# Kernel tuning notes

Hardware: AMD Instinct MI355X
Metric: run time of the kernel (lower is better)

## Reference

```python
import jax, jax.numpy as jnp
import numpy as np

KS = 4
STRIDE = 2
PAD = 1
PI = 3.14  # module uses 3.14, not math.pi


def gabor_filters(freq, theta, psi, sigma):
    # freq/theta/psi/sigma: [O, I] -> weight [O, I, KS, KS]
    x0 = float(np.ceil(KS / 2))  # 2.0 for KS=4
    lin = jnp.linspace(-x0 + 1.0, x0, KS)  # [-1, 0, 1, 2]
    y = lin[:, None]  # varies along kernel dim 0 (meshgrid 'ij')
    x = lin[None, :]  # varies along kernel dim 1
    f = freq[..., None, None]
    t = theta[..., None, None]
    p = psi[..., None, None]
    s = sigma[..., None, None]
    rotx = x * jnp.cos(t) + y * jnp.sin(t)
    roty = -x * jnp.sin(t) + y * jnp.cos(t)
    g = jnp.exp(-0.5 * (rotx ** 2 + roty ** 2) / (s + 0.001) ** 2)
    g = g * jnp.cos(f * rotx + p)
    return g / (2.0 * PI * s ** 2)


def setup_inputs() -> dict:
    key = jax.random.key(0)
    ks = jax.random.split(key, 5)
    B, I, O, H, W = 32, 64, 128, 128, 128
    x = jax.random.normal(ks[0], (B, I, H, W), dtype=jnp.float32)
    # parameter init mirroring the torch module
    freq = (PI / 2) * 1.41 ** (-jax.random.randint(ks[1], (O, I), 0, 5).astype(jnp.float32))
    theta = (PI / 8) * jax.random.randint(ks[2], (O, I), 0, 8).astype(jnp.float32)
    psi = PI * jax.random.uniform(ks[3], (O, I), dtype=jnp.float32)
    sigma = PI / freq
    gamma = jnp.ones((O,), dtype=jnp.float32)
    beta = jnp.zeros((O,), dtype=jnp.float32)
    return {"x": x, "freq": freq, "theta": theta, "psi": psi,
            "sigma": sigma, "gamma": gamma, "beta": beta}


def reference(x, freq, theta, psi, sigma, gamma, beta):
    w = gabor_filters(freq, theta, psi, sigma)  # [O, I, 4, 4]
    out = jax.lax.conv_general_dilated(
        x, w, window_strides=(STRIDE, STRIDE),
        padding=[(PAD, PAD), (PAD, PAD)],
        dimension_numbers=("NCHW", "OIHW", "NCHW"))
    # BatchNorm2d in training mode: batch stats over (N, H, W), eps=1e-5
    mean = jnp.mean(out, axis=(0, 2, 3), keepdims=True)
    var = jnp.var(out, axis=(0, 2, 3), keepdims=True)
    xhat = (out - mean) * jax.lax.rsqrt(var + 1e-5)
    out = gamma[None, :, None, None] * xhat + beta[None, :, None, None]
    # LeakyReLU(0.1)
    return jnp.where(out >= 0, out, 0.1 * out)
```

## Files before the change

kernel.cpp:

```cpp
#include <hip/hip_runtime.h>
#include <hip/hip_bf16.h>

#define BATCH 32
#define CIN   64
#define COUT  128
#define HIN   128
#define WIN   128
#define HOUT  64
#define WOUT  64

typedef unsigned int u32;
typedef __attribute__((ext_vector_type(8))) short short8;
typedef __attribute__((ext_vector_type(4))) float f32x4;


__device__ inline unsigned short f2bf(float v) {
  __hip_bfloat16 h = __float2bfloat16(v);
  return *reinterpret_cast<unsigned short*>(&h);
}
__device__ inline u32 pack2(float a, float b) {
  return (u32)f2bf(a) | ((u32)f2bf(b) << 16);
}

__global__ __launch_bounds__(256) void gabor_kernel(
    const float* __restrict__ freq, const float* __restrict__ theta,
    const float* __restrict__ psi,  const float* __restrict__ sigma,
    __hip_bfloat16* __restrict__ wsw) {
  int idx = blockIdx.x * 256 + threadIdx.x;
  int o = idx >> 6, i = idx & 63;
  float f = freq[idx], t = theta[idx], p = psi[idx], s = sigma[idx];
  float ct = cosf(t), st = sinf(t);
  float se = s + 0.001f;
  float gsc = -0.5f / (se * se);
  float nrm = 1.0f / (2.0f * 3.14f * s * s);
  const float lin[4] = {-1.f, 0.f, 1.f, 2.f};
  int chunk = i >> 2;
  #pragma unroll
  for (int ky = 0; ky < 4; ++ky) {
    #pragma unroll
    for (int kx = 0; kx < 4; ++kx) {
      float xx = lin[kx], yy = lin[ky];
      float rx =  xx * ct + yy * st;
      float ry = -xx * st + yy * ct;
      float g = __expf(gsc * (rx * rx + ry * ry)) * cosf(f * rx + p) * nrm;
      int k6 = (i & 3) * 16 + ky * 4 + kx;
      int sub = 4 * (k6 >> 5) + ((k6 >> 3) & 3);
      int j = k6 & 7;
      int slot = sub ^ (o & 7);
      wsw[(chunk * 16384 + o * 128 + slot * 16 + j * 2) >> 1] = __float2bfloat16(g);
    }
  }
}

constexpr int XPITCH = 70;
constexpr int XROWS  = 18;
constexpr int XCH    = 1260;
constexpr int XBYTES = 20160;
constexpr int NSLOT  = 2304;

__global__ __launch_bounds__(1024, 4) void conv_mfma(
    const float* __restrict__ x, const char* __restrict__ wsW,
    float* __restrict__ out, float2* __restrict__ part) {
  __shared__ __align__(16) char lds[73088];

  const int tid = threadIdx.x;
  const int l = tid & 63, w = tid >> 6;
  const int wm = w & 1, wn = w >> 1;
  const int t4 = l >> 4, lcol = l & 15;
  const int khp = t4 & 1, ihalf = t4 >> 1;
  const int ohb = blockIdx.x, b = blockIdx.y;
  const int oh0 = ohb * 8;

  bool act[3]; int xbyte[3]; const float* gp[3];
  #pragma unroll
  for (int u = 0; u < 3; ++u) {
    int sg = tid + u * 1024;
    int r = sg >> 5, s = sg & 31;
    int ch = r / XROWS, row = r - ch * XROWS;
    int ih = oh0 * 2 - 1 + row;
    act[u] = (sg < NSLOT) && ((unsigned)ih < 128u);
    xbyte[u] = (ch * XCH + row * XPITCH) * 4 + s * 8;
    gp[u] = x + (((size_t)(b * 64 + ch) << 14) + (size_t)ih * 128 + 4 * s);
  }

  float4 xv[3];
  auto XLOAD = [&](int c) {
    #pragma unroll
    for (int u = 0; u < 3; ++u)
      if (act[u]) xv[u] = *(const float4*)(gp[u] + (size_t)c * 65536);
  };
  auto XWRITE = [&](int nb) {
    char* X = lds + 32768 + nb * XBYTES;
    #pragma unroll
    for (int u = 0; u < 3; ++u)
      if (act[u]) {
        char* pb = X + xbyte[u];
        *(unsigned short*)(pb + 6)  = f2bf(xv[u].x);
        *(u32*)(pb + 8)             = pack2(xv[u].y, xv[u].z);
        *(unsigned short*)(pb + 12) = f2bf(xv[u].w);
      }
  };

  auto ASTAGE = [&](int c, int nb) {
    const char* src = wsW + c * 16384 + w * 1024 + l * 16;
    char* dst = lds + nb * 16384 + w * 1024;
    __builtin_amdgcn_global_load_lds(
        (const __attribute__((address_space(1))) u32*)src,
        (__attribute__((address_space(3))) u32*)dst, 16, 0, 0);
  };

  {
    u32* X = (u32*)(lds + 32768);
    for (int i = tid; i < 2 * XBYTES / 4; i += 1024) X[i] = 0;
  }

  f32x4 acc[4][4];
  #pragma unroll
  for (int mf = 0; mf < 4; ++mf)
    #pragma unroll
    for (int nf = 0; nf < 4; ++nf) acc[mf][nf] = {0.f, 0.f, 0.f, 0.f};

  int bo[4];
  #pragma unroll
  for (int nf = 0; nf < 4; ++nf) {
    int nfb = 4 * wn + nf;
    bo[nf] = ihalf * XCH + khp * (2 * XPITCH) + lcol + 1 +
             (nfb >> 2) * (2 * XPITCH) + ((nfb & 3) << 4);
  }

  int ao[4][2];
  #pragma unroll
  for (int mf = 0; mf < 4; ++mf)
    #pragma unroll
    for (int kk = 0; kk < 2; ++kk)
      ao[mf][kk] = (wm * 64 + mf * 16 + lcol) * 128 +
                   (((4 * kk + t4) ^ (lcol & 7)) << 4);

  auto COMPUTE = [&](int cb) {
    const char* Ab = lds + cb * 16384;
    const u32* Xb = (const u32*)(lds + 32768 + cb * XBYTES);
    __builtin_amdgcn_s_setprio(1);
    #pragma unroll
    for (int kk = 0; kk < 2; ++kk) {
      short8 af[4];
      #pragma unroll
      for (int mf = 0; mf < 4; ++mf)
        af[mf] = *(const short8*)(Ab + ao[mf][kk]);
      #pragma unroll
      for (int nf = 0; nf < 4; ++nf) {
        const u32* p = Xb + bo[nf] + kk * (2 * XCH);
        union { u32 u[4]; short8 s8; } bu;
        bu.u[0] = p[0]; bu.u[1] = p[1];
        bu.u[2] = p[XPITCH]; bu.u[3] = p[XPITCH + 1];
        short8 bf = bu.s8;
        #pragma unroll
        for (int mf = 0; mf < 4; ++mf)
          acc[mf][nf] = __builtin_amdgcn_mfma_f32_16x16x32_bf16(af[mf], bf, acc[mf][nf], 0, 0, 0);
      }
    }
    __builtin_amdgcn_s_setprio(0);
  };

  ASTAGE(0, 0); XLOAD(0);
  __syncthreads();
  XWRITE(0);
  __syncthreads();
  for (int c = 0; c < 16; ++c) {
    int cur = c & 1;
    if (c < 15) { ASTAGE(c + 1, cur ^ 1); XLOAD(c + 1); }
    COMPUTE(cur);
    if (c < 15) XWRITE(cur ^ 1);
    __syncthreads();
  }

  size_t obase = ((size_t)b * 128) * 4096;
  #pragma unroll
  for (int mf = 0; mf < 4; ++mf)
    #pragma unroll
    for (int nf = 0; nf < 4; ++nf) {
      int nfb = 4 * wn + nf;
      int oh = oh0 + (nfb >> 2), ow = ((nfb & 3) << 4) + lcol;
      #pragma unroll
      for (int r = 0; r < 4; ++r) {
        int o = wm * 64 + mf * 16 + t4 * 4 + r;
        out[obase + (size_t)o * 4096 + oh * 64 + ow] = acc[mf][nf][r];
      }
    }

  float* ps = (float*)lds;
  #pragma unroll
  for (int mf = 0; mf < 4; ++mf)
    #pragma unroll
    for (int r = 0; r < 4; ++r) {
      float s1 = 0.f, s2 = 0.f;
      #pragma unroll
      for (int nf = 0; nf < 4; ++nf) { float v = acc[mf][nf][r]; s1 += v; s2 += v * v; }
      #pragma unroll
      for (int d = 1; d < 16; d <<= 1) { s1 += __shfl_xor(s1, d); s2 += __shfl_xor(s2, d); }
      if (lcol == 0) {
        int o = wm * 64 + mf * 16 + t4 * 4 + r;
        ps[o * 16 + wn * 2 + 0] = s1;
        ps[o * 16 + wn * 2 + 1] = s2;
      }
    }
  __syncthreads();
  if (tid < 128) {
    float s1 = 0.f, s2 = 0.f;
    #pragma unroll
    for (int q = 0; q < 8; ++q) {
      s1 += ps[tid * 16 + q * 2 + 0];
      s2 += ps[tid * 16 + q * 2 + 1];
    }
    part[(size_t)tid * 256 + b * 8 + ohb] = make_float2(s1, s2);
  }
}

__global__ __launch_bounds__(256) void stats_kernel(
    const float2* __restrict__ part, const float* __restrict__ gamma,
    const float* __restrict__ beta, float2* __restrict__ ab) {
  int o = blockIdx.x;
  int tid = threadIdx.x;
  float2 p = part[(size_t)o * 256 + tid];
  float s1 = p.x, s2 = p.y;
  __shared__ float r1[256], r2[256];
  r1[tid] = s1; r2[tid] = s2;
  __syncthreads();
  for (int off = 128; off > 0; off >>= 1) {
    if (tid < off) { r1[tid] += r1[tid + off]; r2[tid] += r2[tid + off]; }
    __syncthreads();
  }
  if (tid == 0) {
    const float N = (float)BATCH * HOUT * WOUT;
    float mean = r1[0] / N;
    float var  = r2[0] / N - mean * mean;
    float inv  = rsqrtf(var + 1e-5f);
    float a = gamma[o] * inv;
    float bb = beta[o] - mean * a;
    ab[o] = make_float2(a, bb);
  }
}

__global__ __launch_bounds__(256) void norm_kernel(
    float* __restrict__ out, const float2* __restrict__ ab) {
  size_t idx = (size_t)blockIdx.x * 256 + threadIdx.x;
  int o = (int)((idx >> 10) & (COUT - 1));
  float2 s = ab[o];
  float4 v = reinterpret_cast<float4*>(out)[idx];
  v.x = fmaf(v.x, s.x, s.y);
  v.y = fmaf(v.y, s.x, s.y);
  v.z = fmaf(v.z, s.x, s.y);
  v.w = fmaf(v.w, s.x, s.y);
  v.x = v.x >= 0.f ? v.x : 0.1f * v.x;
  v.y = v.y >= 0.f ? v.y : 0.1f * v.y;
  v.z = v.z >= 0.f ? v.z : 0.1f * v.z;
  v.w = v.w >= 0.f ? v.w : 0.1f * v.w;
  reinterpret_cast<float4*>(out)[idx] = v;
}

extern "C" void kernel_launch(void* const* d_in, const int* in_sizes, int n_in,
                              void* d_out, int out_size, void* d_ws, size_t ws_size,
                              hipStream_t stream) {
  const float* x     = (const float*)d_in[0];
  const float* freq  = (const float*)d_in[1];
  const float* theta = (const float*)d_in[2];
  const float* psi   = (const float*)d_in[3];
  const float* sigma = (const float*)d_in[4];
  const float* gamma = (const float*)d_in[5];
  const float* beta  = (const float*)d_in[6];
  float* out = (float*)d_out;

  __hip_bfloat16* wsw = (__hip_bfloat16*)d_ws;
  float2* part = (float2*)((char*)d_ws + 262144);
  float2* ab   = (float2*)((char*)d_ws + 786432);

  gabor_kernel<<<32, 256, 0, stream>>>(freq, theta, psi, sigma, wsw);
  conv_mfma<<<dim3(8, BATCH), 1024, 0, stream>>>(x, (const char*)d_ws, out, part);
  stats_kernel<<<COUT, 256, 0, stream>>>(part, gamma, beta, ab);
  norm_kernel<<<4194304 / 256, 256, 0, stream>>>(out, ab);
}
```

Baseline: 77.28 us.

## Fuse batchnorm stats and normalization into conv kernel via grid-wide barriers

Keeps the conv accumulators in registers and uses two atomic-counter grid barriers to reduce per-channel stats, then writes normalized LeakyReLU output directly. Removes the separate stats and norm kernels and the extra full read/write pass over the output tensor. Relies on all 256 blocks being co-resident; otherwise the spin barriers could deadlock, and the barriers add synchronization latency.

```diff
diff --git a/kernel.cpp b/kernel.cpp
--- a/kernel.cpp
+++ b/kernel.cpp
@@ -22,10 +22,21 @@
   return (u32)f2bf(a) | ((u32)f2bf(b) << 16);
 }
 
+__device__ inline void grid_sync(u32* cnt, u32 target) {
+  __syncthreads();
+  if (threadIdx.x == 0) {
+    __hip_atomic_fetch_add(cnt, 1u, __ATOMIC_RELEASE, __HIP_MEMORY_SCOPE_AGENT);
+    while (__hip_atomic_load(cnt, __ATOMIC_ACQUIRE, __HIP_MEMORY_SCOPE_AGENT) < target)
+      __builtin_amdgcn_s_sleep(2);
+  }
+  __syncthreads();
+}
+
 __global__ __launch_bounds__(256) void gabor_kernel(
     const float* __restrict__ freq, const float* __restrict__ theta,
     const float* __restrict__ psi,  const float* __restrict__ sigma,
-    __hip_bfloat16* __restrict__ wsw) {
+    __hip_bfloat16* __restrict__ wsw, u32* __restrict__ cnt) {
+  if (blockIdx.x == 0 && threadIdx.x == 0) { cnt[0] = 0; cnt[1] = 0; }
   int idx = blockIdx.x * 256 + threadIdx.x;
   int o = idx >> 6, i = idx & 63;
   float f = freq[idx], t = theta[idx], p = psi[idx], s = sigma[idx];
@@ -58,9 +69,11 @@
 constexpr int XBYTES = 20160;
 constexpr int NSLOT  = 2304;
 
-__global__ __launch_bounds__(1024, 4) void conv_mfma(
+__global__ __launch_bounds__(1024, 4) void conv_fused(
     const float* __restrict__ x, const char* __restrict__ wsW,
-    float* __restrict__ out, float2* __restrict__ part) {
+    const float* __restrict__ gamma, const float* __restrict__ beta,
+    float* __restrict__ out, float2* __restrict__ part,
+    u32* __restrict__ cnt, float2* __restrict__ ab) {
   __shared__ __align__(16) char lds[73088];
 
   const int tid = threadIdx.x;
@@ -173,20 +186,6 @@
     __syncthreads();
   }
 
-  size_t obase = ((size_t)b * 128) * 4096;
-  #pragma unroll
-  for (int mf = 0; mf < 4; ++mf)
-    #pragma unroll
-    for (int nf = 0; nf < 4; ++nf) {
-      int nfb = 4 * wn + nf;
-      int oh = oh0 + (nfb >> 2), ow = ((nfb & 3) << 4) + lcol;
-      #pragma unroll
-      for (int r = 0; r < 4; ++r) {
-        int o = wm * 64 + mf * 16 + t4 * 4 + r;
-        out[obase + (size_t)o * 4096 + oh * 64 + ow] = acc[mf][nf][r];
-      }
-    }
-
   float* ps = (float*)lds;
   #pragma unroll
   for (int mf = 0; mf < 4; ++mf)
@@ -213,48 +212,57 @@
     }
     part[(size_t)tid * 256 + b * 8 + ohb] = make_float2(s1, s2);
   }
-}
-
-__global__ __launch_bounds__(256) void stats_kernel(
-    const float2* __restrict__ part, const float* __restrict__ gamma,
-    const float* __restrict__ beta, float2* __restrict__ ab) {
-  int o = blockIdx.x;
-  int tid = threadIdx.x;
-  float2 p = part[(size_t)o * 256 + tid];
-  float s1 = p.x, s2 = p.y;
-  __shared__ float r1[256], r2[256];
-  r1[tid] = s1; r2[tid] = s2;
-  __syncthreads();
-  for (int off = 128; off > 0; off >>= 1) {
-    if (tid < off) { r1[tid] += r1[tid + off]; r2[tid] += r2[tid + off]; }
+
+  grid_sync(&cnt[0], 256);
+
+  const int bid = b * 8 + ohb;
+  if (bid < 128) {
+    float s1 = 0.f, s2 = 0.f;
+    if (tid < 256) {
+      float2 pv = part[(size_t)bid * 256 + tid];
+      s1 = pv.x; s2 = pv.y;
+    }
+    #pragma unroll
+    for (int d = 1; d < 64; d <<= 1) { s1 += __shfl_xor(s1, d); s2 += __shfl_xor(s2, d); }
+    float* psum = (float*)lds;
+    if (l == 0 && w < 4) { psum[w * 2] = s1; psum[w * 2 + 1] = s2; }
     __syncthreads();
-  }
-  if (tid == 0) {
-    const float N = (float)BATCH * HOUT * WOUT;
-    float mean = r1[0] / N;
-    float var  = r2[0] / N - mean * mean;
-    float inv  = rsqrtf(var + 1e-5f);
-    float a = gamma[o] * inv;
-    float bb = beta[o] - mean * a;
-    ab[o] = make_float2(a, bb);
-  }
-}
-
-__global__ __launch_bounds__(256) void norm_kernel(
-    float* __restrict__ out, const float2* __restrict__ ab) {
-  size_t idx = (size_t)blockIdx.x * 256 + threadIdx.x;
-  int o = (int)((idx >> 10) & (COUT - 1));
-  float2 s = ab[o];
-  float4 v = reinterpret_cast<float4*>(out)[idx];
-  v.x = fmaf(v.x, s.x, s.y);
-  v.y = fmaf(v.y, s.x, s.y);
-  v.z = fmaf(v.z, s.x, s.y);
-  v.w = fmaf(v.w, s.x, s.y);
-  v.x = v.x >= 0.f ? v.x : 0.1f * v.x;
-  v.y = v.y >= 0.f ? v.y : 0.1f * v.y;
-  v.z = v.z >= 0.f ? v.z : 0.1f * v.z;
-  v.w = v.w >= 0.f ? v.w : 0.1f * v.w;
-  reinterpret_cast<float4*>(out)[idx] = v;
+    if (tid == 0) {
+      float t1 = 0.f, t2 = 0.f;
+      #pragma unroll
+      for (int q = 0; q < 4; ++q) { t1 += psum[q * 2]; t2 += psum[q * 2 + 1]; }
+      const float N = (float)BATCH * HOUT * WOUT;
+      float mean = t1 / N;
+      float var  = t2 / N - mean * mean;
+      float inv  = rsqrtf(var + 1e-5f);
+      float a  = gamma[bid] * inv;
+      float bb = beta[bid] - mean * a;
+      ab[bid] = make_float2(a, bb);
+    }
+  }
+
+  grid_sync(&cnt[1], 256);
+
+  float2* abl = (float2*)(lds + 1024);
+  if (tid < 128) abl[tid] = ab[tid];
+  __syncthreads();
+
+  size_t obase = ((size_t)b * 128) * 4096;
+  #pragma unroll
+  for (int mf = 0; mf < 4; ++mf)
+    #pragma unroll
+    for (int nf = 0; nf < 4; ++nf) {
+      int nfb = 4 * wn + nf;
+      int oh = oh0 + (nfb >> 2), ow = ((nfb & 3) << 4) + lcol;
+      #pragma unroll
+      for (int r = 0; r < 4; ++r) {
+        int o = wm * 64 + mf * 16 + t4 * 4 + r;
+        float2 s = abl[o];
+        float v = fmaf(acc[mf][nf][r], s.x, s.y);
+        v = v >= 0.f ? v : 0.1f * v;
+        out[obase + (size_t)o * 4096 + oh * 64 + ow] = v;
+      }
+    }
 }
 
 extern "C" void kernel_launch(void* const* d_in, const int* in_sizes, int n_in,
@@ -271,10 +279,10 @@
 
   __hip_bfloat16* wsw = (__hip_bfloat16*)d_ws;
   float2* part = (float2*)((char*)d_ws + 262144);
-  float2* ab   = (float2*)((char*)d_ws + 786432);
-
-  gabor_kernel<<<32, 256, 0, stream>>>(freq, theta, psi, sigma, wsw);
-  conv_mfma<<<dim3(8, BATCH), 1024, 0, stream>>>(x, (const char*)d_ws, out, part);
-  stats_kernel<<<COUT, 256, 0, stream>>>(part, gamma, beta, ab);
-  norm_kernel<<<4194304 / 256, 256, 0, stream>>>(out, ab);
-}
+  u32*    cnt  = (u32*)((char*)d_ws + 524288);
+  float2* ab   = (float2*)((char*)d_ws + 524352);
+
+  gabor_kernel<<<32, 256, 0, stream>>>(freq, theta, psi, sigma, wsw, cnt);
+  conv_fused<<<dim3(8, BATCH), 1024, 0, stream>>>(
+      x, (const char*)d_ws, gamma, beta, out, part, cnt, ab);
+}
```

New measurement: 89.28 us. 15.5% more time.

## Interleave channel pairs in LDS input tile for wider fragment loads

Applied to the files above, without the earlier changes.

Changes the shared-memory layout of the input tile so that two adjacent input channels are packed as bf16 pairs in each 32-bit word, and reorders the Gabor weight K-ordering to match. B-fragment reads become two 8-byte loads instead of four 4-byte loads, and each thread now loads two channels per slot, which cuts the slot count and per-thread index math. This trades a different LDS bank access pattern and a reworked weight swizzle for fewer LDS instructions; the K-ordering must stay consistent between the weight packer and the consumer.

```diff
diff --git a/kernel.cpp b/kernel.cpp
--- a/kernel.cpp
+++ b/kernel.cpp
@@ -34,7 +34,7 @@
   float gsc = -0.5f / (se * se);
   float nrm = 1.0f / (2.0f * 3.14f * s * s);
   const float lin[4] = {-1.f, 0.f, 1.f, 2.f};
-  int chunk = i >> 2;
+  int chunk = i >> 2, i4 = i & 3;
   #pragma unroll
   for (int ky = 0; ky < 4; ++ky) {
     #pragma unroll
@@ -43,61 +43,68 @@
       float rx =  xx * ct + yy * st;
       float ry = -xx * st + yy * ct;
       float g = __expf(gsc * (rx * rx + ry * ry)) * cosf(f * rx + p) * nrm;
-      int k6 = (i & 3) * 16 + ky * 4 + kx;
-      int sub = 4 * (k6 >> 5) + ((k6 >> 3) & 3);
-      int j = k6 & 7;
+      int sub = 4 * (i4 >> 1) + ky;
+      int j = 2 * kx + (i4 & 1);
       int slot = sub ^ (o & 7);
       wsw[(chunk * 16384 + o * 128 + slot * 16 + j * 2) >> 1] = __float2bfloat16(g);
     }
   }
 }
 
-constexpr int XPITCH = 70;
+constexpr int XRLEN  = 136;
 constexpr int XROWS  = 18;
-constexpr int XCH    = 1260;
-constexpr int XBYTES = 20160;
-constexpr int NSLOT  = 2304;
+constexpr int XPLANE = 2448;
+constexpr int XBYTES = 19584;
+constexpr int NSLOT  = 1152;
 
 __global__ __launch_bounds__(1024, 4) void conv_mfma(
     const float* __restrict__ x, const char* __restrict__ wsW,
     float* __restrict__ out, float2* __restrict__ part) {
-  __shared__ __align__(16) char lds[73088];
+  __shared__ __align__(16) char lds[71936];
 
   const int tid = threadIdx.x;
   const int l = tid & 63, w = tid >> 6;
   const int wm = w & 1, wn = w >> 1;
   const int t4 = l >> 4, lcol = l & 15;
-  const int khp = t4 & 1, ihalf = t4 >> 1;
   const int ohb = blockIdx.x, b = blockIdx.y;
   const int oh0 = ohb * 8;
 
-  bool act[3]; int xbyte[3]; const float* gp[3];
-  #pragma unroll
-  for (int u = 0; u < 3; ++u) {
+  bool act[2]; int xdw[2]; const float* gpA[2];
+  #pragma unroll
+  for (int u = 0; u < 2; ++u) {
     int sg = tid + u * 1024;
-    int r = sg >> 5, s = sg & 31;
-    int ch = r / XROWS, row = r - ch * XROWS;
-    int ih = oh0 * 2 - 1 + row;
+    int p = sg / 576, rem = sg - p * 576;
+    int r = rem >> 5, s = rem & 31;
+    int ih = oh0 * 2 - 1 + r;
     act[u] = (sg < NSLOT) && ((unsigned)ih < 128u);
-    xbyte[u] = (ch * XCH + row * XPITCH) * 4 + s * 8;
-    gp[u] = x + (((size_t)(b * 64 + ch) << 14) + (size_t)ih * 128 + 4 * s);
-  }
-
-  float4 xv[3];
+    xdw[u] = p * XPLANE + r * XRLEN + 4 * s + 3;
+    int ch = 2 * p;
+    gpA[u] = x + (((size_t)(b * 64 + ch) << 14) + (size_t)ih * 128 + 4 * s);
+  }
+
+  float4 xva[2], xvb[2];
   auto XLOAD = [&](int c) {
     #pragma unroll
-    for (int u = 0; u < 3; ++u)
-      if (act[u]) xv[u] = *(const float4*)(gp[u] + (size_t)c * 65536);
+    for (int u = 0; u < 2; ++u)
+      if (act[u]) {
+        const float* p = gpA[u] + (size_t)c * 65536;
+        xva[u] = *(const float4*)p;
+        xvb[u] = *(const float4*)(p + 16384);
+      }
   };
   auto XWRITE = [&](int nb) {
-    char* X = lds + 32768 + nb * XBYTES;
-    #pragma unroll
-    for (int u = 0; u < 3; ++u)
+    u32* X = (u32*)(lds + 32768 + nb * XBYTES);
+    #pragma unroll
+    for (int u = 0; u < 2; ++u)
       if (act[u]) {
-        char* pb = X + xbyte[u];
-        *(unsigned short*)(pb + 6)  = f2bf(xv[u].x);
-        *(u32*)(pb + 8)             = pack2(xv[u].y, xv[u].z);
-        *(unsigned short*)(pb + 12) = f2bf(xv[u].w);
+        u32 w0 = pack2(xva[u].x, xvb[u].x);
+        u32 w1 = pack2(xva[u].y, xvb[u].y);
+        u32 w2 = pack2(xva[u].z, xvb[u].z);
+        u32 w3 = pack2(xva[u].w, xvb[u].w);
+        X[xdw[u]] = w0;
+        uint2 mid; mid.x = w1; mid.y = w2;
+        *(uint2*)(X + xdw[u] + 1) = mid;
+        X[xdw[u] + 3] = w3;
       }
   };
 
@@ -124,8 +131,8 @@
   #pragma unroll
   for (int nf = 0; nf < 4; ++nf) {
     int nfb = 4 * wn + nf;
-    bo[nf] = ihalf * XCH + khp * (2 * XPITCH) + lcol + 1 +
-             (nfb >> 2) * (2 * XPITCH) + ((nfb & 3) << 4);
+    int owt = ((nfb & 3) << 4) + lcol;
+    bo[nf] = (2 * (nfb >> 2) + t4) * XRLEN + 2 * owt + 2;
   }
 
   int ao[4][2];
@@ -148,10 +155,10 @@
         af[mf] = *(const short8*)(Ab + ao[mf][kk]);
       #pragma unroll
       for (int nf = 0; nf < 4; ++nf) {
-        const u32* p = Xb + bo[nf] + kk * (2 * XCH);
-        union { u32 u[4]; short8 s8; } bu;
-        bu.u[0] = p[0]; bu.u[1] = p[1];
-        bu.u[2] = p[XPITCH]; bu.u[3] = p[XPITCH + 1];
+        const u32* q = Xb + bo[nf] + kk * XPLANE;
+        union { uint2 u2[2]; short8 s8; } bu;
+        bu.u2[0] = *(const uint2*)(q);
+        bu.u2[1] = *(const uint2*)(q + 2);
         short8 bf = bu.s8;
         #pragma unroll
         for (int mf = 0; mf < 4; ++mf)
```

Result: no change. 77.84 us (+0.7%).
